# Kernel tuning notes

Hardware: AMD Instinct MI355X
Metric: run time of the kernel (lower is better)

The kernel has to match this reference:

```python
import jax, jax.numpy as jnp
import numpy as np

B, S, E = 2, 2048, 2048
H, KVH = 16, 4
D = E // H            # 128
N_REP = H // KVH      # 4


def setup_inputs() -> dict:
    key = jax.random.key(0)
    ks = jax.random.split(key, 5)
    x = jax.random.normal(ks[0], (B, S, E), dtype=jnp.float32)
    # kaiming-normal-ish linear weights, torch layout [out_features, in_features]
    wq_w = jax.random.normal(ks[1], (H * D, E), dtype=jnp.float32) * (2.0 / E) ** 0.5
    wk_w = jax.random.normal(ks[2], (KVH * D, E), dtype=jnp.float32) * (2.0 / E) ** 0.5
    wv_w = jax.random.normal(ks[3], (KVH * D, E), dtype=jnp.float32) * (2.0 / E) ** 0.5
    wo_w = jax.random.normal(ks[4], (E, E), dtype=jnp.float32) * (2.0 / E) ** 0.5
    # standard RoPE frequencies: theta = 10000
    inv_freq = 1.0 / (10000.0 ** (np.arange(0, D, 2, dtype=np.float32) / D))  # [D/2]
    t = np.arange(S, dtype=np.float32)
    ang = np.outer(t, inv_freq)  # [S, D/2]
    freqs_cos = jnp.asarray(np.cos(ang), dtype=jnp.float32)
    freqs_sin = jnp.asarray(np.sin(ang), dtype=jnp.float32)
    return {"x": x, "wq_w": wq_w, "wk_w": wk_w, "wv_w": wv_w, "wo_w": wo_w,
            "freqs_cos": freqs_cos, "freqs_sin": freqs_sin, "start_pos": 0}


def _rope(t, cos, sin):
    # t: [B, S, h, D]; cos/sin: [S, D/2] -> complex multiply on (even, odd) pairs
    tr = t.reshape(*t.shape[:-1], -1, 2)
    xr, xi = tr[..., 0], tr[..., 1]
    c = cos[None, :, None, :]
    s = sin[None, :, None, :]
    orr = xr * c - xi * s
    oi = xr * s + xi * c
    return jnp.stack([orr, oi], axis=-1).reshape(t.shape)


def reference(x, wq_w, wk_w, wv_w, wo_w, freqs_cos, freqs_sin, start_pos):
    b, s, e = x.shape
    q = jnp.einsum('bse,fe->bsf', x, wq_w).reshape(b, s, H, D)
    k = jnp.einsum('bse,fe->bsf', x, wk_w).reshape(b, s, KVH, D)
    v = jnp.einsum('bse,fe->bsf', x, wv_w).reshape(b, s, KVH, D)
    q = _rope(q, freqs_cos, freqs_sin)
    k = _rope(k, freqs_cos, freqs_sin)
    # faithful to torch .repeat(1,1,n_rep,1): TILE kv heads -> head h uses kv head h % KVH
    k = jnp.tile(k, (1, 1, N_REP, 1))  # [b, s, H, D]
    v = jnp.tile(v, (1, 1, N_REP, 1))
    q = q.transpose(0, 2, 1, 3)  # [b, H, s, D]
    k = k.transpose(0, 2, 1, 3)
    v = v.transpose(0, 2, 1, 3)
    scores = jnp.einsum('bhqd,bhkd->bhqk', q, k) * (1.0 / D ** 0.5)
    causal = jnp.tril(jnp.ones((s, s), dtype=bool))
    scores = jnp.where(causal[None, None], scores, -jnp.inf)
    attn = jax.nn.softmax(scores, axis=-1)
    out = jnp.einsum('bhqk,bhkd->bhqd', attn, v)
    out = out.transpose(0, 2, 1, 3).reshape(b, s, e)
    return jnp.einsum('bse,fe->bsf', out, wo_w)
```

## Files before the change

kernel.cpp:

```cpp
#include <hip/hip_runtime.h>
#include <hip/hip_bf16.h>

typedef unsigned short u16;
typedef unsigned int u32;
typedef short bf16x8 __attribute__((ext_vector_type(8)));
typedef float f32x4 __attribute__((ext_vector_type(4)));

#define MFMA_BF16 __builtin_amdgcn_mfma_f32_16x16x32_bf16

#define B_   2
#define S_   2048
#define E_   2048
#define H_   16
#define KVH_ 4
#define D_   128
#define M_   (B_ * S_)
#define NQKV 3072
#define SCALE_ 0.08838834764831845f

__device__ __forceinline__ float b2f(u16 u) {
    union { u32 i; float f; } x; x.i = ((u32)u) << 16; return x.f;
}
__device__ __forceinline__ u16 f2b(float f) {
    __hip_bfloat16 h = __float2bfloat16(f);
    return *reinterpret_cast<u16*>(&h);
}

__device__ __forceinline__ void async16(const u16* g, u16* l) {
    __builtin_amdgcn_global_load_lds(
        (const __attribute__((address_space(1))) void*)g,
        (__attribute__((address_space(3))) void*)l, 16, 0, 0);
}

__device__ __forceinline__ uint4 pack8(const float* p) {
    float4 a = *reinterpret_cast<const float4*>(p);
    float4 b = *reinterpret_cast<const float4*>(p + 4);
    union { uint4 v; u16 h[8]; } pk;
    pk.h[0] = f2b(a.x); pk.h[1] = f2b(a.y); pk.h[2] = f2b(a.z); pk.h[3] = f2b(a.w);
    pk.h[4] = f2b(b.x); pk.h[5] = f2b(b.y); pk.h[6] = f2b(b.z); pk.h[7] = f2b(b.w);
    return pk.v;
}

__global__ __launch_bounds__(256)
void conv4(const float* __restrict__ s0, u16* __restrict__ d0, int n0,
           const float* __restrict__ s1, u16* __restrict__ d1, int n1,
           const float* __restrict__ s2, u16* __restrict__ d2, int n2,
           const float* __restrict__ s3, u16* __restrict__ d3) {
    int bid = blockIdx.x;
    const float* s; u16* d; size_t base;
    if (bid < n0)                { s = s0; d = d0; base = (size_t)bid * 2048; }
    else if (bid < n0 + n1)      { s = s1; d = d1; base = (size_t)(bid - n0) * 2048; }
    else if (bid < n0 + n1 + n2) { s = s2; d = d2; base = (size_t)(bid - n0 - n1) * 2048; }
    else                         { s = s3; d = d3; base = (size_t)(bid - n0 - n1 - n2) * 2048; }
    size_t i = base + (size_t)threadIdx.x * 8;
    *reinterpret_cast<uint4*>(d + i) = pack8(s + i);
}

template <int NREP>
__device__ __forceinline__ void gemm_core(const u16* __restrict__ Ag, int m0,
                                          const u16* const (&Bp)[NREP],
                                          u16* lds, f32x4 (&acc)[4][NREP]) {
    constexpr int BUFSZ = 8192 + NREP * 4096;
    const int tid = threadIdx.x, wave = tid >> 6, lane = tid & 63;
    const int l15 = lane & 15, quad = lane >> 4;
    const int wm = wave & 1, wn = wave >> 1;

    const f32x4 zero4 = {0.f, 0.f, 0.f, 0.f};
    #pragma unroll
    for (int i = 0; i < 4; ++i)
        #pragma unroll
        for (int j = 0; j < NREP; ++j) acc[i][j] = zero4;

    const u16* Ap[2];
    #pragma unroll
    for (int j = 0; j < 2; ++j) {
        int tA = wave * 2 + j;
        Ap[j] = Ag + (size_t)(m0 + (tA >> 1) * 16 + l15) * E_
                   + (tA & 1) * 32 + quad * 8;
    }

    auto stage = [&](int p, int kt) {
        #pragma unroll
        for (int j = 0; j < 2; ++j)
            async16(Ap[j] + kt, &lds[p * BUFSZ + (wave * 2 + j) * 512]);
        #pragma unroll
        for (int j = 0; j < NREP; ++j)
            async16(Bp[j] + kt, &lds[p * BUFSZ + 8192 + (wave * NREP + j) * 512]);
    };

    stage(0, 0);

    int p = 0;
    for (int kt = 0; kt < E_; kt += 64) {
        __builtin_amdgcn_s_barrier();
        if (kt + 64 < E_) {
            stage(p ^ 1, kt + 64);
            if constexpr (NREP == 2)
                asm volatile("s_waitcnt vmcnt(4)" ::: "memory");
            else
                asm volatile("s_waitcnt vmcnt(5)" ::: "memory");
        } else {
            asm volatile("s_waitcnt vmcnt(0)" ::: "memory");
        }
        __builtin_amdgcn_sched_barrier(0);
        __builtin_amdgcn_s_barrier();
        __builtin_amdgcn_sched_barrier(0);

        #pragma unroll
        for (int kb = 0; kb < 2; ++kb) {
            bf16x8 bfr[NREP];
            #pragma unroll
            for (int ni = 0; ni < NREP; ++ni)
                bfr[ni] = *reinterpret_cast<const bf16x8*>(
                    &lds[p * BUFSZ + 8192 +
                         ((((wn * NREP + ni) << 1) | kb) << 9) + lane * 8]);
            bf16x8 af[4];
            #pragma unroll
            for (int i = 0; i < 4; ++i)
                af[i] = *reinterpret_cast<const bf16x8*>(
                    &lds[p * BUFSZ + ((((wm * 4 + i) << 1) | kb) << 9) + lane * 8]);
            __builtin_amdgcn_s_setprio(1);
            #pragma unroll
            for (int mi = 0; mi < 4; ++mi)
                #pragma unroll
                for (int ni = 0; ni < NREP; ++ni)
                    acc[mi][ni] = MFMA_BF16(af[mi], bfr[ni], acc[mi][ni], 0, 0, 0);
            __builtin_amdgcn_s_setprio(0);
        }
        p ^= 1;
    }
}

__device__ __forceinline__ void xcd_swz512(int lin, int& nIdx, int& mIdx) {
    const int xcd = lin & 7, c = lin >> 3;
    nIdx = (xcd & 3) * 4 + (c & 3);
    mIdx = (xcd >> 2) * 16 + (c >> 2);
}

__global__ __launch_bounds__(512, 4)
void qkv_rope_gemm(const u16* __restrict__ xb, const u16* __restrict__ wqb,
                   const u16* __restrict__ wkb, const u16* __restrict__ wvb,
                   const float* __restrict__ fc, const float* __restrict__ fs,
                   u16* __restrict__ Qr, u16* __restrict__ Kr,
                   u16* __restrict__ VrT) {
    __shared__ __align__(16) u16 lds[2 * (8192 + 12288)];
    const int tid = threadIdx.x, wave = tid >> 6, lane = tid & 63;
    const int l15 = lane & 15, quad = lane >> 4;
    int nIdx, mIdx;
    xcd_swz512(blockIdx.y * gridDim.x + blockIdx.x, nIdx, mIdx);
    const int m0 = mIdx * 128, n0 = nIdx * 192;

    const u16* Bp[3];
    #pragma unroll
    for (int j = 0; j < 3; ++j) {
        int tB = wave * 3 + j;
        int n = n0 + (tB >> 1) * 16 + l15;
        const u16* base; int nl;
        if (n < 2048)      { base = wqb; nl = n; }
        else if (n < 2560) { base = wkb; nl = n - 2048; }
        else               { base = wvb; nl = n - 2560; }
        Bp[j] = base + (size_t)nl * E_ + (tB & 1) * 32 + quad * 8;
    }

    f32x4 acc[4][3];
    gemm_core<3>(xb, m0, Bp, lds, acc);

    const int wm = wave & 1, wn = wave >> 1;
    const int mb_ = m0 + wm * 64, nbase = n0 + wn * 48;
    #pragma unroll
    for (int mi = 0; mi < 4; ++mi)
        #pragma unroll
        for (int ni = 0; ni < 3; ++ni) {
            const int ngrp = nbase + ni * 16;
            if (ngrp >= 2560) {
                const int nv = ngrp + l15 - 2560;
                const int kh = nv >> 7, dd = nv & 127;
                const int mr = mb_ + mi * 16 + quad * 4;
                const int b = mr >> 11, s0 = mr & 2047;
                u16 w[4];
                #pragma unroll
                for (int r = 0; r < 4; ++r) w[r] = f2b(acc[mi][ni][r]);
                *reinterpret_cast<uint2*>(
                    VrT + ((size_t)(b * KVH_ + kh) * D_ + dd) * S_ + s0) =
                    *reinterpret_cast<const uint2*>(w);
            } else {
                #pragma unroll
                for (int r = 0; r < 4; ++r) {
                    int m = mb_ + mi * 16 + quad * 4 + r;
                    int n = ngrp + l15;
                    int b = m >> 11, s = m & 2047;
                    float v = acc[mi][ni][r];
                    float other = __shfl_xor(v, 1);
                    int d = n & 127;
                    int fi = s * 64 + (d >> 1);
                    float c  = fc[fi];
                    float sn = fs[fi];
                    v = (n & 1) ? (other * sn + v * c) : (v * c - other * sn);
                    if (n < 2048) {
                        Qr[((size_t)(b * H_ + (n >> 7)) * S_ + s) * D_ + d] = f2b(v);
                    } else {
                        int kh = (n - 2048) >> 7;
                        Kr[((size_t)(b * KVH_ + kh) * S_ + s) * D_ + d] = f2b(v);
                    }
                }
            }
        }
}

__global__ __launch_bounds__(1024, 4)
void flash2(const u16* __restrict__ Qr, const u16* __restrict__ Kr,
            const u16* __restrict__ VrT, u16* __restrict__ AO) {
    __shared__ __align__(16) u16 Ks[2][2][8192];
    __shared__ __align__(16) u16 Vs[2][2][8192];
    const int tid = threadIdx.x, wave = tid >> 6, lane = tid & 63;
    const int grp = wave >> 3, gw = wave & 7;
    const int l15 = lane & 15, quad = lane >> 4;
    const int lin = blockIdx.x;
    const int qt  = 15 - (lin >> 5);
    const int sub = lin & 31;
    const int h = sub & 15, b = sub >> 4;
    const int kvh = h & 3;
    const u16* Qb = Qr + (size_t)(b * H_ + h) * S_ * D_;
    const u16* Kb = Kr + (size_t)(b * KVH_ + kvh) * S_ * D_;
    const u16* Vb = VrT + (size_t)(b * KVH_ + kvh) * D_ * S_;
    const int q0 = qt * 128 + gw * 16;
    const int qg = q0 + l15;

    bf16x8 bq[4];
    #pragma unroll
    for (int kk = 0; kk < 4; ++kk)
        bq[kk] = *reinterpret_cast<const bf16x8*>(
            Qb + (size_t)qg * D_ + kk * 32 + quad * 8);

    f32x4 o[8];
    const f32x4 zero4 = {0.f, 0.f, 0.f, 0.f};
    #pragma unroll
    for (int i = 0; i < 8; ++i) o[i] = zero4;
    float m_i = -__builtin_inff(), l_i = 0.f;

    const int nt = qt + 1;
    const int tbase = grp ? nt : 0;
    const int f0 = gw * 2, f1 = gw * 2 + 1;
    const u16* kp0 = Kb + (size_t)tbase * 64 * D_ +
        (size_t)((f0 >> 2) * 16 + l15) * D_ + (f0 & 3) * 32 + quad * 8;
    const u16* kp1 = Kb + (size_t)tbase * 64 * D_ +
        (size_t)((f1 >> 2) * 16 + l15) * D_ + (f1 & 3) * 32 + quad * 8;
    const u16* vp0 = Vb + (size_t)tbase * 64 +
        (size_t)((f0 >> 1) * 16 + l15) * S_ + (f0 & 1) * 32 + quad * 8;
    const u16* vp1 = Vb + (size_t)tbase * 64 +
        (size_t)((f1 >> 1) * 16 + l15) * S_ + (f1 & 1) * 32 + quad * 8;

    async16(kp0, &Ks[grp][0][f0 * 512]);
    async16(kp1, &Ks[grp][0][f1 * 512]);
    async16(vp0, &Vs[grp][0][f0 * 512]);
    async16(vp1, &Vs[grp][0][f1 * 512]);

    int p = 0;
    for (int i = 0; i < nt; ++i) {
        __builtin_amdgcn_s_barrier();
        if (i + 1 < nt) {
            size_t ko = (size_t)(i + 1) * 64 * D_;
            size_t vo = (size_t)(i + 1) * 64;
            async16(kp0 + ko, &Ks[grp][p ^ 1][f0 * 512]);
            async16(kp1 + ko, &Ks[grp][p ^ 1][f1 * 512]);
            async16(vp0 + vo, &Vs[grp][p ^ 1][f0 * 512]);
            async16(vp1 + vo, &Vs[grp][p ^ 1][f1 * 512]);
            asm volatile("s_waitcnt vmcnt(4)" ::: "memory");
        } else {
            asm volatile("s_waitcnt vmcnt(0)" ::: "memory");
        }
        __builtin_amdgcn_sched_barrier(0);
        __builtin_amdgcn_s_barrier();
        __builtin_amdgcn_sched_barrier(0);

        const int kvbase = (tbase + i) * 64;
        if (q0 + 15 >= kvbase) {
            f32x4 st[4];
            #pragma unroll
            for (int kb = 0; kb < 4; ++kb) st[kb] = zero4;
            __builtin_amdgcn_s_setprio(1);
            #pragma unroll
            for (int kk = 0; kk < 4; ++kk)
                #pragma unroll
                for (int kb = 0; kb < 4; ++kb) {
                    bf16x8 ak = *reinterpret_cast<const bf16x8*>(
                        &Ks[grp][p][(((kb << 2) | kk) << 9) + lane * 8]);
                    st[kb] = MFMA_BF16(ak, bq[kk], st[kb], 0, 0, 0);
                }
            __builtin_amdgcn_s_setprio(0);

            float mx = -__builtin_inff();
            if (kvbase + 63 > q0) {
                #pragma unroll
                for (int kb = 0; kb < 4; ++kb)
                    #pragma unroll
                    for (int r = 0; r < 4; ++r) {
                        float s = st[kb][r] * SCALE_;
                        if (kvbase + kb * 16 + quad * 4 + r > qg)
                            s = -__builtin_inff();
                        st[kb][r] = s;
                        mx = fmaxf(mx, s);
                    }
            } else {
                #pragma unroll
                for (int kb = 0; kb < 4; ++kb)
                    #pragma unroll
                    for (int r = 0; r < 4; ++r) {
                        float s = st[kb][r] * SCALE_;
                        st[kb][r] = s;
                        mx = fmaxf(mx, s);
                    }
            }
            mx = fmaxf(mx, __shfl_xor(mx, 16));
            mx = fmaxf(mx, __shfl_xor(mx, 32));
            const bool nodefer = !__all(mx - m_i <= 8.0f);
            float mnew = nodefer ? fmaxf(m_i, mx) : m_i;
            float a = __expf(m_i - mnew);
            float sum = 0.f;
            #pragma unroll
            for (int kb = 0; kb < 4; ++kb)
                #pragma unroll
                for (int r = 0; r < 4; ++r) {
                    float pv = __expf(st[kb][r] - mnew);
                    st[kb][r] = pv;
                    sum += pv;
                }
            sum += __shfl_xor(sum, 16);
            sum += __shfl_xor(sum, 32);
            l_i = l_i * a + sum;
            m_i = mnew;
            if (nodefer) {
                #pragma unroll
                for (int mi = 0; mi < 8; ++mi)
                    #pragma unroll
                    for (int r = 0; r < 4; ++r) o[mi][r] *= a;
            }

            #pragma unroll
            for (int kf = 0; kf < 2; ++kf) {
                u32 pk[4];
                #pragma unroll
                for (int r = 0; r < 4; ++r)
                    pk[r] = (u32)f2b(st[kf * 2 + 0][r]) |
                            ((u32)f2b(st[kf * 2 + 1][r]) << 16);
                bf16x8 bp;
                u16* bh = (u16*)&bp;
                #pragma unroll
                for (int j2 = 0; j2 < 8; ++j2) {
                    int src = ((quad & 1) * 2 + (j2 >> 2)) * 16 + l15;
                    u32 v = __shfl((int)pk[j2 & 3], src);
                    bh[j2] = (lane >= 32) ? (u16)(v >> 16) : (u16)v;
                }
                __builtin_amdgcn_s_setprio(1);
                #pragma unroll
                for (int mi = 0; mi < 8; ++mi) {
                    bf16x8 av = *reinterpret_cast<const bf16x8*>(
                        &Vs[grp][p][(((mi << 1) | kf) << 9) + lane * 8]);
                    o[mi] = MFMA_BF16(av, bp, o[mi], 0, 0, 0);
                }
                __builtin_amdgcn_s_setprio(0);
            }
        }
        p ^= 1;
    }

    float* shf = (float*)&Ks[0][0][0];
    float* shm = (float*)&Vs[0][0][0];
    __syncthreads();
    if (grp == 1) {
        #pragma unroll
        for (int mi = 0; mi < 8; ++mi)
            #pragma unroll
            for (int r = 0; r < 4; ++r)
                shf[((mi << 2) | r) * 512 + gw * 64 + lane] = o[mi][r];
        shm[gw * 64 + lane] = m_i;
        shm[512 + gw * 64 + lane] = l_i;
    }
    __syncthreads();
    if (grp == 0) {
        float m1 = shm[gw * 64 + lane];
        float l1 = shm[512 + gw * 64 + lane];
        float M  = fmaxf(m_i, m1);
        float w0 = __expf(m_i - M), w1 = __expf(m1 - M);
        float inv = 1.0f / (w0 * l_i + w1 * l1);
        size_t base = ((size_t)(b * S_ + qg)) * E_ + h * D_;
        #pragma unroll
        for (int mi = 0; mi < 8; ++mi) {
            u16 w[4];
            #pragma unroll
            for (int r = 0; r < 4; ++r) {
                float ov = w0 * o[mi][r] +
                           w1 * shf[((mi << 2) | r) * 512 + gw * 64 + lane];
                w[r] = f2b(ov * inv);
            }
            *reinterpret_cast<uint2*>(AO + base + mi * 16 + quad * 4) =
                *reinterpret_cast<const uint2*>(w);
        }
    }
}

__global__ __launch_bounds__(512, 4)
void out_proj_gemm(const u16* __restrict__ ao, const u16* __restrict__ wob,
                   float* __restrict__ out) {
    __shared__ __align__(16) u16 lds[2 * (8192 + 8192)];
    const int tid = threadIdx.x, wave = tid >> 6, lane = tid & 63;
    const int l15 = lane & 15, quad = lane >> 4;
    int nIdx, mIdx;
    xcd_swz512(blockIdx.y * gridDim.x + blockIdx.x, nIdx, mIdx);
    const int m0 = mIdx * 128, n0 = nIdx * 128;

    const u16* Bp[2];
    #pragma unroll
    for (int j = 0; j < 2; ++j) {
        int tB = wave * 2 + j;
        Bp[j] = wob + (size_t)(n0 + (tB >> 1) * 16 + l15) * E_
                    + (tB & 1) * 32 + quad * 8;
    }

    f32x4 acc[4][2];
    gemm_core<2>(ao, m0, Bp, lds, acc);

    const int wm = wave & 1, wn = wave >> 1;
    const int mb_ = m0 + wm * 64, nbase = n0 + wn * 32;
    #pragma unroll
    for (int mi = 0; mi < 4; ++mi)
        #pragma unroll
        for (int ni = 0; ni < 2; ++ni)
            #pragma unroll
            for (int r = 0; r < 4; ++r) {
                int m = mb_ + mi * 16 + quad * 4 + r;
                int n = nbase + ni * 16 + l15;
                out[(size_t)m * E_ + n] = acc[mi][ni][r];
            }
}

extern "C" void kernel_launch(void* const* d_in, const int* in_sizes, int n_in,
                              void* d_out, int out_size, void* d_ws, size_t ws_size,
                              hipStream_t stream) {
    const float* x  = (const float*)d_in[0];
    const float* wq = (const float*)d_in[1];
    const float* wk = (const float*)d_in[2];
    const float* wv = (const float*)d_in[3];
    const float* wo = (const float*)d_in[4];
    const float* fc = (const float*)d_in[5];
    const float* fs = (const float*)d_in[6];
    float* out = (float*)d_out;

    u16* wqb = (u16*)d_ws;
    u16* xb  = wqb + 4194304;
    u16* Qr  = wqb + 12582912;
    u16* Kr  = wqb + 20971520;
    u16* VrT = wqb + 23068672;
    u16* wob = wqb;
    u16* AO  = xb;
    u16* wkb = (u16*)d_out;
    u16* wvb = wkb + 1048576;

    conv4<<<7168, 256, 0, stream>>>(x, xb, 4096, wq, wqb, 2048,
                                    wk, wkb, 512, wv, wvb);
    qkv_rope_gemm<<<dim3(NQKV / 192, M_ / 128), 512, 0, stream>>>(
        xb, wqb, wkb, wvb, fc, fs, Qr, Kr, VrT);
    flash2<<<dim3(512), 1024, 0, stream>>>(Qr, Kr, VrT, AO);
    conv4<<<2048, 256, 0, stream>>>(wo, wob, 2048, nullptr, nullptr, 0,
                                    nullptr, nullptr, 0, nullptr, nullptr);
    out_proj_gemm<<<dim3(E_ / 128, M_ / 128), 512, 0, stream>>>(AO, wob, out);
}
```

Measured before the change: 341.3 us.

## Load GEMM B operands and attention K/V directly from global into registers

The GEMM core now stages only the A tile through LDS and loads each wave's B fragments straight from global memory into registers, double-buffered with the main loop unrolled by two. The flash attention kernel drops its LDS staging of K and V and reads them directly from global/L2 into registers right before the MFMAs. This removes LDS traffic and some barriers, and shrinks LDS so more blocks can fit per CU. In exchange, B and K/V data that several waves share is re-read from cache by each wave, and global load latency is no longer hidden by async prefetch in the attention kernel.

```diff
diff --git a/kernel.cpp b/kernel.cpp
--- a/kernel.cpp
+++ b/kernel.cpp
@@ -58,12 +58,11 @@
 
 template <int NREP>
 __device__ __forceinline__ void gemm_core(const u16* __restrict__ Ag, int m0,
-                                          const u16* const (&Bp)[NREP],
+                                          const u16* const (&Bw)[NREP],
                                           u16* lds, f32x4 (&acc)[4][NREP]) {
-    constexpr int BUFSZ = 8192 + NREP * 4096;
     const int tid = threadIdx.x, wave = tid >> 6, lane = tid & 63;
     const int l15 = lane & 15, quad = lane >> 4;
-    const int wm = wave & 1, wn = wave >> 1;
+    const int wm = wave & 1;
 
     const f32x4 zero4 = {0.f, 0.f, 0.f, 0.f};
     #pragma unroll
@@ -79,55 +78,64 @@
                    + (tA & 1) * 32 + quad * 8;
     }
 
-    auto stage = [&](int p, int kt) {
+    auto stageA = [&](int p, int kt) {
         #pragma unroll
         for (int j = 0; j < 2; ++j)
-            async16(Ap[j] + kt, &lds[p * BUFSZ + (wave * 2 + j) * 512]);
-        #pragma unroll
-        for (int j = 0; j < NREP; ++j)
-            async16(Bp[j] + kt, &lds[p * BUFSZ + 8192 + (wave * NREP + j) * 512]);
+            async16(Ap[j] + kt, &lds[p * 8192 + (wave * 2 + j) * 512]);
     };
-
-    stage(0, 0);
-
-    int p = 0;
-    for (int kt = 0; kt < E_; kt += 64) {
-        __builtin_amdgcn_s_barrier();
-        if (kt + 64 < E_) {
-            stage(p ^ 1, kt + 64);
-            if constexpr (NREP == 2)
-                asm volatile("s_waitcnt vmcnt(4)" ::: "memory");
-            else
-                asm volatile("s_waitcnt vmcnt(5)" ::: "memory");
-        } else {
-            asm volatile("s_waitcnt vmcnt(0)" ::: "memory");
+    auto loadB = [&](bf16x8 (&bs)[NREP][2], int kt) {
+        #pragma unroll
+        for (int ni = 0; ni < NREP; ++ni)
+            #pragma unroll
+            for (int kb = 0; kb < 2; ++kb)
+                bs[ni][kb] = *reinterpret_cast<const bf16x8*>(
+                    Bw[ni] + kt + kb * 32);
+    };
+    auto compute = [&](int p, bf16x8 (&bs)[NREP][2]) {
+        #pragma unroll
+        for (int kb = 0; kb < 2; ++kb) {
+            bf16x8 af[4];
+            #pragma unroll
+            for (int i = 0; i < 4; ++i)
+                af[i] = *reinterpret_cast<const bf16x8*>(
+                    &lds[p * 8192 + ((((wm * 4 + i) << 1) | kb) << 9) + lane * 8]);
+            __builtin_amdgcn_s_setprio(1);
+            #pragma unroll
+            for (int mi = 0; mi < 4; ++mi)
+                #pragma unroll
+                for (int ni = 0; ni < NREP; ++ni)
+                    acc[mi][ni] = MFMA_BF16(af[mi], bs[ni][kb], acc[mi][ni], 0, 0, 0);
+            __builtin_amdgcn_s_setprio(0);
         }
+    };
+    auto waitN = [&]() {
+        if constexpr (NREP == 2) asm volatile("s_waitcnt vmcnt(6)" ::: "memory");
+        else                     asm volatile("s_waitcnt vmcnt(8)" ::: "memory");
         __builtin_amdgcn_sched_barrier(0);
         __builtin_amdgcn_s_barrier();
         __builtin_amdgcn_sched_barrier(0);
-
-        #pragma unroll
-        for (int kb = 0; kb < 2; ++kb) {
-            bf16x8 bfr[NREP];
-            #pragma unroll
-            for (int ni = 0; ni < NREP; ++ni)
-                bfr[ni] = *reinterpret_cast<const bf16x8*>(
-                    &lds[p * BUFSZ + 8192 +
-                         ((((wn * NREP + ni) << 1) | kb) << 9) + lane * 8]);
-            bf16x8 af[4];
-            #pragma unroll
-            for (int i = 0; i < 4; ++i)
-                af[i] = *reinterpret_cast<const bf16x8*>(
-                    &lds[p * BUFSZ + ((((wm * 4 + i) << 1) | kb) << 9) + lane * 8]);
-            __builtin_amdgcn_s_setprio(1);
-            #pragma unroll
-            for (int mi = 0; mi < 4; ++mi)
-                #pragma unroll
-                for (int ni = 0; ni < NREP; ++ni)
-                    acc[mi][ni] = MFMA_BF16(af[mi], bfr[ni], acc[mi][ni], 0, 0, 0);
-            __builtin_amdgcn_s_setprio(0);
+    };
+
+    bf16x8 b0[NREP][2], b1[NREP][2];
+    stageA(0, 0); loadB(b0, 0);
+
+    int p = 0;
+    for (int kt = 0; kt < E_; kt += 128) {
+        __builtin_amdgcn_s_barrier();
+        stageA(p ^ 1, kt + 64); loadB(b1, kt + 64);
+        waitN();
+        compute(p, b0); p ^= 1;
+        __builtin_amdgcn_s_barrier();
+        if (kt + 128 < E_) {
+            stageA(p ^ 1, kt + 128); loadB(b0, kt + 128);
+            waitN();
+        } else {
+            asm volatile("s_waitcnt vmcnt(0)" ::: "memory");
+            __builtin_amdgcn_sched_barrier(0);
+            __builtin_amdgcn_s_barrier();
+            __builtin_amdgcn_sched_barrier(0);
         }
-        p ^= 1;
+        compute(p, b1); p ^= 1;
     }
 }
 
@@ -143,29 +151,29 @@
                    const float* __restrict__ fc, const float* __restrict__ fs,
                    u16* __restrict__ Qr, u16* __restrict__ Kr,
                    u16* __restrict__ VrT) {
-    __shared__ __align__(16) u16 lds[2 * (8192 + 12288)];
+    __shared__ __align__(16) u16 lds[2 * 8192];
     const int tid = threadIdx.x, wave = tid >> 6, lane = tid & 63;
     const int l15 = lane & 15, quad = lane >> 4;
+    const int wn = wave >> 1;
     int nIdx, mIdx;
     xcd_swz512(blockIdx.y * gridDim.x + blockIdx.x, nIdx, mIdx);
     const int m0 = mIdx * 128, n0 = nIdx * 192;
 
-    const u16* Bp[3];
-    #pragma unroll
-    for (int j = 0; j < 3; ++j) {
-        int tB = wave * 3 + j;
-        int n = n0 + (tB >> 1) * 16 + l15;
+    const u16* Bw[3];
+    #pragma unroll
+    for (int ni = 0; ni < 3; ++ni) {
+        int n = n0 + (wn * 3 + ni) * 16 + l15;
         const u16* base; int nl;
         if (n < 2048)      { base = wqb; nl = n; }
         else if (n < 2560) { base = wkb; nl = n - 2048; }
         else               { base = wvb; nl = n - 2560; }
-        Bp[j] = base + (size_t)nl * E_ + (tB & 1) * 32 + quad * 8;
+        Bw[ni] = base + (size_t)nl * E_ + quad * 8;
     }
 
     f32x4 acc[4][3];
-    gemm_core<3>(xb, m0, Bp, lds, acc);
-
-    const int wm = wave & 1, wn = wave >> 1;
+    gemm_core<3>(xb, m0, Bw, lds, acc);
+
+    const int wm = wave & 1;
     const int mb_ = m0 + wm * 64, nbase = n0 + wn * 48;
     #pragma unroll
     for (int mi = 0; mi < 4; ++mi)
@@ -210,8 +218,8 @@
 __global__ __launch_bounds__(1024, 4)
 void flash2(const u16* __restrict__ Qr, const u16* __restrict__ Kr,
             const u16* __restrict__ VrT, u16* __restrict__ AO) {
-    __shared__ __align__(16) u16 Ks[2][2][8192];
-    __shared__ __align__(16) u16 Vs[2][2][8192];
+    __shared__ float shf[16384];
+    __shared__ float shm[1024];
     const int tid = threadIdx.x, wave = tid >> 6, lane = tid & 63;
     const int grp = wave >> 3, gw = wave & 7;
     const int l15 = lane & 15, quad = lane >> 4;
@@ -238,56 +246,32 @@
     for (int i = 0; i < 8; ++i) o[i] = zero4;
     float m_i = -__builtin_inff(), l_i = 0.f;
 
+    const u16* Kp = Kb + (size_t)l15 * D_ + quad * 8;
+    const u16* Vp = Vb + (size_t)l15 * S_ + quad * 8;
+
     const int nt = qt + 1;
     const int tbase = grp ? nt : 0;
-    const int f0 = gw * 2, f1 = gw * 2 + 1;
-    const u16* kp0 = Kb + (size_t)tbase * 64 * D_ +
-        (size_t)((f0 >> 2) * 16 + l15) * D_ + (f0 & 3) * 32 + quad * 8;
-    const u16* kp1 = Kb + (size_t)tbase * 64 * D_ +
-        (size_t)((f1 >> 2) * 16 + l15) * D_ + (f1 & 3) * 32 + quad * 8;
-    const u16* vp0 = Vb + (size_t)tbase * 64 +
-        (size_t)((f0 >> 1) * 16 + l15) * S_ + (f0 & 1) * 32 + quad * 8;
-    const u16* vp1 = Vb + (size_t)tbase * 64 +
-        (size_t)((f1 >> 1) * 16 + l15) * S_ + (f1 & 1) * 32 + quad * 8;
-
-    async16(kp0, &Ks[grp][0][f0 * 512]);
-    async16(kp1, &Ks[grp][0][f1 * 512]);
-    async16(vp0, &Vs[grp][0][f0 * 512]);
-    async16(vp1, &Vs[grp][0][f1 * 512]);
-
-    int p = 0;
+
     for (int i = 0; i < nt; ++i) {
         __builtin_amdgcn_s_barrier();
-        if (i + 1 < nt) {
-            size_t ko = (size_t)(i + 1) * 64 * D_;
-            size_t vo = (size_t)(i + 1) * 64;
-            async16(kp0 + ko, &Ks[grp][p ^ 1][f0 * 512]);
-            async16(kp1 + ko, &Ks[grp][p ^ 1][f1 * 512]);
-            async16(vp0 + vo, &Vs[grp][p ^ 1][f0 * 512]);
-            async16(vp1 + vo, &Vs[grp][p ^ 1][f1 * 512]);
-            asm volatile("s_waitcnt vmcnt(4)" ::: "memory");
-        } else {
-            asm volatile("s_waitcnt vmcnt(0)" ::: "memory");
-        }
-        __builtin_amdgcn_sched_barrier(0);
-        __builtin_amdgcn_s_barrier();
-        __builtin_amdgcn_sched_barrier(0);
-
         const int kvbase = (tbase + i) * 64;
         if (q0 + 15 >= kvbase) {
             f32x4 st[4];
             #pragma unroll
             for (int kb = 0; kb < 4; ++kb) st[kb] = zero4;
-            __builtin_amdgcn_s_setprio(1);
-            #pragma unroll
-            for (int kk = 0; kk < 4; ++kk)
-                #pragma unroll
-                for (int kb = 0; kb < 4; ++kb) {
-                    bf16x8 ak = *reinterpret_cast<const bf16x8*>(
-                        &Ks[grp][p][(((kb << 2) | kk) << 9) + lane * 8]);
-                    st[kb] = MFMA_BF16(ak, bq[kk], st[kb], 0, 0, 0);
-                }
-            __builtin_amdgcn_s_setprio(0);
+            #pragma unroll
+            for (int kk = 0; kk < 4; ++kk) {
+                bf16x8 ak[4];
+                #pragma unroll
+                for (int kb = 0; kb < 4; ++kb)
+                    ak[kb] = *reinterpret_cast<const bf16x8*>(
+                        Kp + (size_t)(kvbase + kb * 16) * D_ + kk * 32);
+                __builtin_amdgcn_s_setprio(1);
+                #pragma unroll
+                for (int kb = 0; kb < 4; ++kb)
+                    st[kb] = MFMA_BF16(ak[kb], bq[kk], st[kb], 0, 0, 0);
+                __builtin_amdgcn_s_setprio(0);
+            }
 
             float mx = -__builtin_inff();
             if (kvbase + 63 > q0) {
@@ -351,21 +335,20 @@
                     u32 v = __shfl((int)pk[j2 & 3], src);
                     bh[j2] = (lane >= 32) ? (u16)(v >> 16) : (u16)v;
                 }
+                bf16x8 av[8];
+                #pragma unroll
+                for (int mi = 0; mi < 8; ++mi)
+                    av[mi] = *reinterpret_cast<const bf16x8*>(
+                        Vp + (size_t)(mi * 16) * S_ + kvbase + kf * 32);
                 __builtin_amdgcn_s_setprio(1);
                 #pragma unroll
-                for (int mi = 0; mi < 8; ++mi) {
-                    bf16x8 av = *reinterpret_cast<const bf16x8*>(
-                        &Vs[grp][p][(((mi << 1) | kf) << 9) + lane * 8]);
-                    o[mi] = MFMA_BF16(av, bp, o[mi], 0, 0, 0);
-                }
+                for (int mi = 0; mi < 8; ++mi)
+                    o[mi] = MFMA_BF16(av[mi], bp, o[mi], 0, 0, 0);
                 __builtin_amdgcn_s_setprio(0);
             }
         }
-        p ^= 1;
-    }
-
-    float* shf = (float*)&Ks[0][0][0];
-    float* shm = (float*)&Vs[0][0][0];
+    }
+
     __syncthreads();
     if (grp == 1) {
         #pragma unroll
@@ -402,25 +385,23 @@
 __global__ __launch_bounds__(512, 4)
 void out_proj_gemm(const u16* __restrict__ ao, const u16* __restrict__ wob,
                    float* __restrict__ out) {
-    __shared__ __align__(16) u16 lds[2 * (8192 + 8192)];
+    __shared__ __align__(16) u16 lds[2 * 8192];
     const int tid = threadIdx.x, wave = tid >> 6, lane = tid & 63;
     const int l15 = lane & 15, quad = lane >> 4;
+    const int wn = wave >> 1;
     int nIdx, mIdx;
     xcd_swz512(blockIdx.y * gridDim.x + blockIdx.x, nIdx, mIdx);
     const int m0 = mIdx * 128, n0 = nIdx * 128;
 
-    const u16* Bp[2];
-    #pragma unroll
-    for (int j = 0; j < 2; ++j) {
-        int tB = wave * 2 + j;
-        Bp[j] = wob + (size_t)(n0 + (tB >> 1) * 16 + l15) * E_
-                    + (tB & 1) * 32 + quad * 8;
-    }
+    const u16* Bw[2];
+    #pragma unroll
+    for (int ni = 0; ni < 2; ++ni)
+        Bw[ni] = wob + (size_t)(n0 + (wn * 2 + ni) * 16 + l15) * E_ + quad * 8;
 
     f32x4 acc[4][2];
-    gemm_core<2>(ao, m0, Bp, lds, acc);
-
-    const int wm = wave & 1, wn = wave >> 1;
+    gemm_core<2>(ao, m0, Bw, lds, acc);
+
+    const int wm = wave & 1;
     const int mb_ = m0 + wm * 64, nbase = n0 + wn * 32;
     #pragma unroll
     for (int mi = 0; mi < 4; ++mi)
```

New measurement: 676.4 us. 98.2% more time.

## Switch projection GEMMs to 256x256 tiles with fine-grained split A/B pipelining

Applied to the files above, without the earlier changes.

Replaces the 128x192 and 128x128 GEMM cores with a 256x256-tile GEMM in which each wave computes 128x64 with 8x4 MFMA accumulators. Staging of A and B is split into separate half-K phases over four LDS slots, interleaving async loads with MFMA work and barriers. The XCD-aware block swizzle is remapped for the new grids. Larger tiles increase operand reuse and cut global/L2 traffic, at the cost of fewer blocks (96 and 64, below the CU count) and more registers and LDS per block.

```diff
diff --git a/kernel.cpp b/kernel.cpp
--- a/kernel.cpp
+++ b/kernel.cpp
@@ -56,121 +56,122 @@
     *reinterpret_cast<uint4*>(d + i) = pack8(s + i);
 }
 
-template <int NREP>
-__device__ __forceinline__ void gemm_core(const u16* __restrict__ Ag, int m0,
-                                          const u16* const (&Bp)[NREP],
-                                          u16* lds, f32x4 (&acc)[4][NREP]) {
-    constexpr int BUFSZ = 8192 + NREP * 4096;
+#define G256_PHASE(PAR, KB, MH, STFN, SP, SS, KCOL, VM)                        \
+    {                                                                          \
+        bf16x8 af[4], bf[4];                                                   \
+        const u16* slot_ = lds + (((PAR) << 1) | (KB)) * 16384;                \
+        _Pragma("unroll")                                                      \
+        for (int i_ = 0; i_ < 4; ++i_)                                         \
+            af[i_] = *reinterpret_cast<const bf16x8*>(                         \
+                slot_ + ((wm * 8 + (MH) * 4 + i_) << 9) + lane * 8);           \
+        _Pragma("unroll")                                                      \
+        for (int n_ = 0; n_ < 4; ++n_)                                         \
+            bf[n_] = *reinterpret_cast<const bf16x8*>(                         \
+                slot_ + 8192 + ((wnn * 4 + n_) << 9) + lane * 8);              \
+        STFN((SP), (SS), (KCOL));                                              \
+        __builtin_amdgcn_sched_barrier(0);                                     \
+        __builtin_amdgcn_s_barrier();                                          \
+        asm volatile("s_waitcnt lgkmcnt(0)" ::: "memory");                     \
+        __builtin_amdgcn_sched_barrier(0);                                     \
+        __builtin_amdgcn_s_setprio(1);                                         \
+        _Pragma("unroll")                                                      \
+        for (int i_ = 0; i_ < 4; ++i_)                                         \
+            _Pragma("unroll")                                                  \
+            for (int n_ = 0; n_ < 4; ++n_)                                     \
+                acc[(MH) * 4 + i_][n_] =                                       \
+                    MFMA_BF16(af[i_], bf[n_], acc[(MH) * 4 + i_][n_], 0, 0, 0);\
+        __builtin_amdgcn_s_setprio(0);                                         \
+        __builtin_amdgcn_sched_barrier(0);                                     \
+        if (VM) asm volatile("s_waitcnt vmcnt(8)" ::: "memory");               \
+        __builtin_amdgcn_sched_barrier(0);                                     \
+        __builtin_amdgcn_s_barrier();                                          \
+        __builtin_amdgcn_sched_barrier(0);                                     \
+    }
+
+__device__ __forceinline__ void gemm256(const u16* __restrict__ Ag,
+                                        const u16* __restrict__ Bg,
+                                        int m0, u16* lds, f32x4 (&acc)[8][4]) {
     const int tid = threadIdx.x, wave = tid >> 6, lane = tid & 63;
     const int l15 = lane & 15, quad = lane >> 4;
-    const int wm = wave & 1, wn = wave >> 1;
+    const int wm = wave >> 2, wnn = wave & 3;
 
     const f32x4 zero4 = {0.f, 0.f, 0.f, 0.f};
     #pragma unroll
-    for (int i = 0; i < 4; ++i)
+    for (int i = 0; i < 8; ++i)
         #pragma unroll
-        for (int j = 0; j < NREP; ++j) acc[i][j] = zero4;
-
-    const u16* Ap[2];
-    #pragma unroll
-    for (int j = 0; j < 2; ++j) {
-        int tA = wave * 2 + j;
-        Ap[j] = Ag + (size_t)(m0 + (tA >> 1) * 16 + l15) * E_
-                   + (tA & 1) * 32 + quad * 8;
+        for (int j = 0; j < 4; ++j) acc[i][j] = zero4;
+
+    const int fA = wave * 2;
+    const u16* aR0 = Ag + (size_t)(m0 + (fA + 0) * 16 + l15) * E_ + quad * 8;
+    const u16* aR1 = Ag + (size_t)(m0 + (fA + 1) * 16 + l15) * E_ + quad * 8;
+    const u16* bR0 = Bg + (size_t)((fA + 0) * 16 + l15) * E_ + quad * 8;
+    const u16* bR1 = Bg + (size_t)((fA + 1) * 16 + l15) * E_ + quad * 8;
+
+    auto stA = [&](int par, int s, int kcol) {
+        u16* dst = lds + (((par) << 1) | (s)) * 16384 + fA * 512;
+        async16(aR0 + kcol, dst);
+        async16(aR1 + kcol, dst + 512);
+    };
+    auto stB = [&](int par, int s, int kcol) {
+        u16* dst = lds + (((par) << 1) | (s)) * 16384 + 8192 + fA * 512;
+        async16(bR0 + kcol, dst);
+        async16(bR1 + kcol, dst + 512);
+    };
+
+    stA(0, 0, 0);   stB(0, 0, 0);
+    stA(0, 1, 32);  stB(0, 1, 32);
+    stA(1, 0, 64);  stB(1, 0, 64);
+    asm volatile("s_waitcnt vmcnt(8)" ::: "memory");
+    __builtin_amdgcn_sched_barrier(0);
+    __builtin_amdgcn_s_barrier();
+    __builtin_amdgcn_sched_barrier(0);
+
+    #pragma unroll 1
+    for (int it = 0; it < E_ / 128; ++it) {
+        const int t  = it * 2;
+        const int k1 = (t + 1) * 64;
+        const int k2 = ((t + 2) * 64 < E_) ? (t + 2) * 64 : E_ - 64;
+        const int k3 = ((t + 3) * 64 < E_) ? (t + 3) * 64 : E_ - 64;
+        G256_PHASE(0, 0, 0, stA, 1, 1, k1 + 32, false)
+        G256_PHASE(0, 0, 1, stB, 1, 1, k1 + 32, true )
+        G256_PHASE(0, 1, 0, stA, 0, 0, k2,      false)
+        G256_PHASE(0, 1, 1, stB, 0, 0, k2,      true )
+        G256_PHASE(1, 0, 0, stA, 0, 1, k2 + 32, false)
+        G256_PHASE(1, 0, 1, stB, 0, 1, k2 + 32, true )
+        G256_PHASE(1, 1, 0, stA, 1, 0, k3,      false)
+        G256_PHASE(1, 1, 1, stB, 1, 0, k3,      true )
     }
-
-    auto stage = [&](int p, int kt) {
-        #pragma unroll
-        for (int j = 0; j < 2; ++j)
-            async16(Ap[j] + kt, &lds[p * BUFSZ + (wave * 2 + j) * 512]);
-        #pragma unroll
-        for (int j = 0; j < NREP; ++j)
-            async16(Bp[j] + kt, &lds[p * BUFSZ + 8192 + (wave * NREP + j) * 512]);
-    };
-
-    stage(0, 0);
-
-    int p = 0;
-    for (int kt = 0; kt < E_; kt += 64) {
-        __builtin_amdgcn_s_barrier();
-        if (kt + 64 < E_) {
-            stage(p ^ 1, kt + 64);
-            if constexpr (NREP == 2)
-                asm volatile("s_waitcnt vmcnt(4)" ::: "memory");
-            else
-                asm volatile("s_waitcnt vmcnt(5)" ::: "memory");
-        } else {
-            asm volatile("s_waitcnt vmcnt(0)" ::: "memory");
-        }
-        __builtin_amdgcn_sched_barrier(0);
-        __builtin_amdgcn_s_barrier();
-        __builtin_amdgcn_sched_barrier(0);
-
-        #pragma unroll
-        for (int kb = 0; kb < 2; ++kb) {
-            bf16x8 bfr[NREP];
-            #pragma unroll
-            for (int ni = 0; ni < NREP; ++ni)
-                bfr[ni] = *reinterpret_cast<const bf16x8*>(
-                    &lds[p * BUFSZ + 8192 +
-                         ((((wn * NREP + ni) << 1) | kb) << 9) + lane * 8]);
-            bf16x8 af[4];
-            #pragma unroll
-            for (int i = 0; i < 4; ++i)
-                af[i] = *reinterpret_cast<const bf16x8*>(
-                    &lds[p * BUFSZ + ((((wm * 4 + i) << 1) | kb) << 9) + lane * 8]);
-            __builtin_amdgcn_s_setprio(1);
-            #pragma unroll
-            for (int mi = 0; mi < 4; ++mi)
-                #pragma unroll
-                for (int ni = 0; ni < NREP; ++ni)
-                    acc[mi][ni] = MFMA_BF16(af[mi], bfr[ni], acc[mi][ni], 0, 0, 0);
-            __builtin_amdgcn_s_setprio(0);
-        }
-        p ^= 1;
-    }
-}
-
-__device__ __forceinline__ void xcd_swz512(int lin, int& nIdx, int& mIdx) {
-    const int xcd = lin & 7, c = lin >> 3;
-    nIdx = (xcd & 3) * 4 + (c & 3);
-    mIdx = (xcd >> 2) * 16 + (c >> 2);
-}
-
-__global__ __launch_bounds__(512, 4)
+}
+
+__global__ __launch_bounds__(512, 2)
 void qkv_rope_gemm(const u16* __restrict__ xb, const u16* __restrict__ wqb,
                    const u16* __restrict__ wkb, const u16* __restrict__ wvb,
                    const float* __restrict__ fc, const float* __restrict__ fs,
                    u16* __restrict__ Qr, u16* __restrict__ Kr,
                    u16* __restrict__ VrT) {
-    __shared__ __align__(16) u16 lds[2 * (8192 + 12288)];
+    __shared__ __align__(16) u16 lds[65536];
     const int tid = threadIdx.x, wave = tid >> 6, lane = tid & 63;
     const int l15 = lane & 15, quad = lane >> 4;
-    int nIdx, mIdx;
-    xcd_swz512(blockIdx.y * gridDim.x + blockIdx.x, nIdx, mIdx);
-    const int m0 = mIdx * 128, n0 = nIdx * 192;
-
-    const u16* Bp[3];
+    const int wm = wave >> 2, wnn = wave & 3;
+    const int lin = blockIdx.y * gridDim.x + blockIdx.x;
+    const int xcd = lin & 7, c = lin >> 3;
+    const int nIdx = (xcd & 1) * 6 + c % 6;
+    const int mIdx = (xcd >> 1) * 4 + c / 6;
+    const int m0 = mIdx * 256, n0 = nIdx * 256;
+
+    const u16* wsel;
+    if (n0 < 2048)      wsel = wqb + (size_t)n0 * E_;
+    else if (n0 < 2560) wsel = wkb + (size_t)(n0 - 2048) * E_;
+    else                wsel = wvb + (size_t)(n0 - 2560) * E_;
+
+    f32x4 acc[8][4];
+    gemm256(xb, wsel, m0, lds, acc);
+
+    const int mb_ = m0 + wm * 128, nbase = n0 + wnn * 64;
     #pragma unroll
-    for (int j = 0; j < 3; ++j) {
-        int tB = wave * 3 + j;
-        int n = n0 + (tB >> 1) * 16 + l15;
-        const u16* base; int nl;
-        if (n < 2048)      { base = wqb; nl = n; }
-        else if (n < 2560) { base = wkb; nl = n - 2048; }
-        else               { base = wvb; nl = n - 2560; }
-        Bp[j] = base + (size_t)nl * E_ + (tB & 1) * 32 + quad * 8;
-    }
-
-    f32x4 acc[4][3];
-    gemm_core<3>(xb, m0, Bp, lds, acc);
-
-    const int wm = wave & 1, wn = wave >> 1;
-    const int mb_ = m0 + wm * 64, nbase = n0 + wn * 48;
-    #pragma unroll
-    for (int mi = 0; mi < 4; ++mi)
+    for (int mi = 0; mi < 8; ++mi)
         #pragma unroll
-        for (int ni = 0; ni < 3; ++ni) {
+        for (int ni = 0; ni < 4; ++ni) {
             const int ngrp = nbase + ni * 16;
             if (ngrp >= 2560) {
                 const int nv = ngrp + l15 - 2560;
@@ -193,9 +194,9 @@
                     float other = __shfl_xor(v, 1);
                     int d = n & 127;
                     int fi = s * 64 + (d >> 1);
-                    float c  = fc[fi];
+                    float cc = fc[fi];
                     float sn = fs[fi];
-                    v = (n & 1) ? (other * sn + v * c) : (v * c - other * sn);
+                    v = (n & 1) ? (other * sn + v * cc) : (v * cc - other * sn);
                     if (n < 2048) {
                         Qr[((size_t)(b * H_ + (n >> 7)) * S_ + s) * D_ + d] = f2b(v);
                     } else {
@@ -399,33 +400,27 @@
     }
 }
 
-__global__ __launch_bounds__(512, 4)
+__global__ __launch_bounds__(512, 2)
 void out_proj_gemm(const u16* __restrict__ ao, const u16* __restrict__ wob,
                    float* __restrict__ out) {
-    __shared__ __align__(16) u16 lds[2 * (8192 + 8192)];
+    __shared__ __align__(16) u16 lds[65536];
     const int tid = threadIdx.x, wave = tid >> 6, lane = tid & 63;
     const int l15 = lane & 15, quad = lane >> 4;
-    int nIdx, mIdx;
-    xcd_swz512(blockIdx.y * gridDim.x + blockIdx.x, nIdx, mIdx);
-    const int m0 = mIdx * 128, n0 = nIdx * 128;
-
-    const u16* Bp[2];
+    const int wm = wave >> 2, wnn = wave & 3;
+    const int lin = blockIdx.y * gridDim.x + blockIdx.x;
+    const int xcd = lin & 7, c = lin >> 3;
+    const int nIdx = (xcd & 1) * 4 + (c & 3);
+    const int mIdx = (xcd >> 1) * 4 + (c >> 2);
+    const int m0 = mIdx * 256, n0 = nIdx * 256;
+
+    f32x4 acc[8][4];
+    gemm256(ao, wob + (size_t)n0 * E_, m0, lds, acc);
+
+    const int mb_ = m0 + wm * 128, nbase = n0 + wnn * 64;
     #pragma unroll
-    for (int j = 0; j < 2; ++j) {
-        int tB = wave * 2 + j;
-        Bp[j] = wob + (size_t)(n0 + (tB >> 1) * 16 + l15) * E_
-                    + (tB & 1) * 32 + quad * 8;
-    }
-
-    f32x4 acc[4][2];
-    gemm_core<2>(ao, m0, Bp, lds, acc);
-
-    const int wm = wave & 1, wn = wave >> 1;
-    const int mb_ = m0 + wm * 64, nbase = n0 + wn * 32;
-    #pragma unroll
-    for (int mi = 0; mi < 4; ++mi)
+    for (int mi = 0; mi < 8; ++mi)
         #pragma unroll
-        for (int ni = 0; ni < 2; ++ni)
+        for (int ni = 0; ni < 4; ++ni)
             #pragma unroll
             for (int r = 0; r < 4; ++r) {
                 int m = mb_ + mi * 16 + quad * 4 + r;
@@ -458,10 +453,10 @@
 
     conv4<<<7168, 256, 0, stream>>>(x, xb, 4096, wq, wqb, 2048,
                                     wk, wkb, 512, wv, wvb);
-    qkv_rope_gemm<<<dim3(NQKV / 192, M_ / 128), 512, 0, stream>>>(
+    qkv_rope_gemm<<<dim3(NQKV / 256, M_ / 256), 512, 0, stream>>>(
         xb, wqb, wkb, wvb, fc, fs, Qr, Kr, VrT);
     flash2<<<dim3(512), 1024, 0, stream>>>(Qr, Kr, VrT, AO);
     conv4<<<2048, 256, 0, stream>>>(wo, wob, 2048, nullptr, nullptr, 0,
                                     nullptr, nullptr, 0, nullptr, nullptr);
-    out_proj_gemm<<<dim3(E_ / 128, M_ / 128), 512, 0, stream>>>(AO, wob, out);
-}
+    out_proj_gemm<<<dim3(E_ / 256, M_ / 256), 512, 0, stream>>>(AO, wob, out);
+}
```

Result: no change. 342.3 us (+0.3%).
